# Performance work log

Hardware: AMD Instinct MI355X
Metric: run time of the kernel (lower is better)

Reference implementation:

```python
import jax, jax.numpy as jnp
import numpy as np


def setup_inputs() -> dict:
    key = jax.random.key(0)
    ks = jax.random.split(key, 5)
    B, S, H, I = 8, 2048, 1024, 4096
    # int8 quantized activation / weights / int8 bias, held as int32 for portability
    hidden_states = jax.random.randint(ks[0], (B, S, H), -128, 128, dtype=jnp.int32)
    w_fc = jax.random.randint(ks[1], (H, I), -128, 128, dtype=jnp.int32)   # Conv1D weight [in, out]
    b_fc = jax.random.randint(ks[2], (I,), -128, 128, dtype=jnp.int32)     # int8 bias (B8)
    w_proj = jax.random.randint(ks[3], (I, H), -128, 128, dtype=jnp.int32)
    b_proj = jax.random.normal(ks[4], (H,), dtype=jnp.float32)             # fp32 bias (BFP32)
    alpha_fc = jnp.float32(0.004)   # (x_scale * w_scale / out_scale) of c_fc
    beta_fc = jnp.float32(0.02)     # bias_scale / out_scale of c_fc
    alpha_proj = jnp.float32(0.003) # x_scale * w_scale of c_proj (dequant to fp32)
    return {
        "hidden_states": hidden_states,
        "w_fc": w_fc, "b_fc": b_fc, "alpha_fc": alpha_fc, "beta_fc": beta_fc,
        "w_proj": w_proj, "b_proj": b_proj, "alpha_proj": alpha_proj,
    }


def reference(hidden_states, w_fc, b_fc, alpha_fc, beta_fc, w_proj, b_proj, alpha_proj):
    # ---- c_fc: W8A8B8O8 Conv1D + fused ReLU + requantization to int8 ----
    acc1 = jnp.matmul(hidden_states, w_fc)                       # [B,S,I] int32
    h = acc1.astype(jnp.float32) * alpha_fc + b_fc.astype(jnp.float32) * beta_fc
    h = jax.nn.relu(h)
    # requantize to int8 (round + saturate)
    h_q = jnp.clip(jnp.round(h), -128.0, 127.0).astype(jnp.int32)  # [B,S,I]
    # ---- c_proj: W8A8BFP32OFP32 Conv1D (dequant to fp32) ----
    acc2 = jnp.matmul(h_q, w_proj)                               # [B,S,H] int32
    out = acc2.astype(jnp.float32) * alpha_proj + b_proj
    # dropout is identity in eval mode
    return out
```

## Files before the change

kernel.cpp:

```cpp
#include <hip/hip_runtime.h>
#include <cstdint>
#include <cstddef>

typedef int int4v __attribute__((ext_vector_type(4)));
typedef signed char schar;

#define DEVI __device__ __forceinline__

DEVI void load_lds16(const void* g, void* l) {
  __builtin_amdgcn_global_load_lds(
      (const __attribute__((address_space(1))) void*)g,
      (__attribute__((address_space(3))) void*)l, 16, 0, 0);
}

#define BAR() __builtin_amdgcn_s_barrier()
#define LGKM0()                                                     \
  do {                                                              \
    asm volatile("s_waitcnt lgkmcnt(0)" ::: "memory");              \
    __builtin_amdgcn_sched_barrier(0);                              \
  } while (0)
#define VMW(n)                                                      \
  do {                                                              \
    asm volatile("s_waitcnt vmcnt(" #n ")" ::: "memory");           \
    __builtin_amdgcn_sched_barrier(0);                              \
  } while (0)

__global__ __launch_bounds__(256) void pack_i8(const int* __restrict__ src,
                                               signed char* __restrict__ dst,
                                               int n4) {
  int i = blockIdx.x * 256 + threadIdx.x;
  if (i >= n4) return;
  int4v v = ((const int4v*)src)[i];
  int p = (v.x & 255) | ((v.y & 255) << 8) | ((v.z & 255) << 16) | (v.w << 24);
  ((int*)dst)[i] = p;
}

__global__ __launch_bounds__(256) void pack_wT(const int* __restrict__ w,
                                               signed char* __restrict__ wT,
                                               int K, int N) {
  __shared__ signed char t[64][68];
  int n0 = blockIdx.x * 64, k0 = blockIdx.y * 64;
  int tr = threadIdx.x >> 6, tc = threadIdx.x & 63;
#pragma unroll
  for (int i = 0; i < 16; ++i) {
    int r = i * 4 + tr;
    t[r][tc] = (signed char)w[(size_t)(k0 + r) * N + n0 + tc];
  }
  __syncthreads();
#pragma unroll
  for (int i = 0; i < 16; ++i) {
    int r = i * 4 + tr;
    wT[(size_t)(n0 + r) * K + k0 + tc] = t[tc][r];
  }
}

template <int EPI>
__global__ __launch_bounds__(512, 2) void gemm8(
    const schar* __restrict__ A, const schar* __restrict__ BT,
    int M, int N, int K, const int* __restrict__ bias_i,
    const float* __restrict__ alphaP, const float* __restrict__ betaP,
    const float* __restrict__ bias_f, schar* __restrict__ outQ,
    float* __restrict__ outF) {
  extern __shared__ schar lds[];
  constexpr int ATILE = 32768;

  const int tid = threadIdx.x;
  const int wid = tid >> 6, lane = tid & 63;
  const int wr = wid >> 2, wc = wid & 3;
  const int l16 = lane & 15, l4 = lane >> 4;

  const int gx = gridDim.x;
  const int nwg = gx * gridDim.y;
  const int bid = blockIdx.y * gx + blockIdx.x;
  const int swz = (bid & 7) * (nwg >> 3) + (bid >> 3);
  const int rowBase = (swz / gx) * 256;
  const int colBase = (swz % gx) * 256;

  const int NT = K >> 7;

  const int off0 = tid * 16, off1 = 8192 + tid * 16;
  const int rl0 = off0 >> 7, rl1 = off1 >> 7;
  const int gs0 = ((off0 >> 4) & 7) ^ (rl0 & 7);
  const int gs1 = ((off1 >> 4) & 7) ^ (rl1 & 7);
  const schar* gA0 = A + (size_t)(rowBase + rl0) * K + gs0 * 16;
  const schar* gA1 = A + (size_t)(rowBase + rl1) * K + gs1 * 16;
  const schar* gB0 = BT + (size_t)(colBase + rl0) * K + gs0 * 16;
  const schar* gB1 = BT + (size_t)(colBase + rl1) * K + gs1 * 16;
  const size_t hstep = (size_t)128 * K;
  const int wb = wid * 1024;

  auto stA = [&](int buf, int t, int h) {
    schar* d = lds + buf * ATILE + h * 16384 + wb;
    load_lds16(gA0 + (size_t)t * 128 + (size_t)h * hstep, d);
    load_lds16(gA1 + (size_t)t * 128 + (size_t)h * hstep, d + 8192);
  };
  auto stB = [&](int buf, int t, int h) {
    schar* d = lds + 2 * ATILE + buf * ATILE + h * 16384 + wb;
    load_lds16(gB0 + (size_t)t * 128 + (size_t)h * hstep, d);
    load_lds16(gB1 + (size_t)t * 128 + (size_t)h * hstep, d + 8192);
  };

  int4v acc[8][4] = {};
  int4v a[4][2], b0[2][2], b1[2][2];

#define LDA(QM, Ab)                                                         \
  do {                                                                      \
    _Pragma("unroll") for (int mi = 0; mi < 4; ++mi)                        \
        _Pragma("unroll") for (int kk = 0; kk < 2; ++kk) a[mi][kk] =        \
        *(const int4v*)((Ab) + (wr * 128 + (QM)*64 + mi * 16 + l16) * 128 + \
                        (((kk * 4) + l4) ^ (l16 & 7)) * 16);                \
  } while (0)
#define LDB(B, QN, Bb)                                                       \
  do {                                                                       \
    _Pragma("unroll") for (int ni = 0; ni < 2; ++ni)                         \
        _Pragma("unroll") for (int kk = 0; kk < 2; ++kk) (B)[ni][kk] =       \
        *(const int4v*)((Bb) +                                               \
                        (wc * 64 + ((QN)*2 + ni) * 16 + l16) * 128 +         \
                        (((kk * 4) + l4) ^ (l16 & 7)) * 16);                 \
  } while (0)
#define MMQ(QM, QN, B)                                                       \
  do {                                                                       \
    __builtin_amdgcn_s_setprio(1);                                           \
    _Pragma("unroll") for (int kk = 0; kk < 2; ++kk)                         \
        _Pragma("unroll") for (int mi = 0; mi < 4; ++mi)                     \
            _Pragma("unroll") for (int ni = 0; ni < 2; ++ni)                 \
                acc[(QM)*4 + mi][(QN)*2 + ni] =                              \
        __builtin_amdgcn_mfma_i32_16x16x64_i8(                               \
            a[mi][kk], (B)[ni][kk], acc[(QM)*4 + mi][(QN)*2 + ni], 0, 0, 0); \
    __builtin_amdgcn_s_setprio(0);                                           \
  } while (0)

  stA(0, 0, 0);
  stA(0, 0, 1);
  stB(0, 0, 0);
  stB(0, 0, 1);
  if (NT > 1) {
    stB(1, 1, 0);
    stB(1, 1, 1);
    VMW(4);
  } else {
    VMW(0);
  }
  BAR();

  for (int T = 0; T < NT; ++T) {
    const int cb = T & 1, ob = cb ^ 1;
    const schar* Ac = lds + cb * ATILE;
    const schar* Bc = lds + 2 * ATILE + cb * ATILE;

    LDA(0, Ac);
    LDB(b0, 0, Bc);
    if (T + 1 < NT) stA(ob, T + 1, 0);
    BAR();
    LGKM0();
    MMQ(0, 0, b0);
    BAR();
    LDB(b1, 1, Bc);
    if (T + 1 < NT) stA(ob, T + 1, 1);
    BAR();
    LGKM0();
    MMQ(0, 1, b1);
    BAR();
    LDA(1, Ac);
    if (T + 2 < NT) stB(cb, T + 2, 0);
    BAR();
    LGKM0();
    MMQ(1, 0, b0);
    BAR();
    if (T + 2 < NT) stB(cb, T + 2, 1);
    BAR();
    MMQ(1, 1, b1);
    if (T + 2 < NT) {
      VMW(4);
    } else if (T + 1 < NT) {
      VMW(0);
    }
    BAR();
  }

  const float alpha = alphaP[0];
  if (EPI == 0) {
    const float beta = betaP[0];
#pragma unroll
    for (int MI = 0; MI < 8; ++MI) {
      int row = rowBase + wr * 128 + MI * 16 + l4 * 4;
#pragma unroll
      for (int NI = 0; NI < 4; ++NI) {
        int col = colBase + wc * 64 + NI * 16 + l16;
        float bt = (float)bias_i[col] * beta;
#pragma unroll
        for (int j = 0; j < 4; ++j) {
          float h = (float)acc[MI][NI][j] * alpha + bt;
          h = fmaxf(h, 0.f);
          h = rintf(h);
          h = fminf(h, 127.f);
          outQ[(size_t)(row + j) * N + col] = (schar)h;
        }
      }
    }
  } else {
#pragma unroll
    for (int MI = 0; MI < 8; ++MI) {
      int row = rowBase + wr * 128 + MI * 16 + l4 * 4;
#pragma unroll
      for (int NI = 0; NI < 4; ++NI) {
        int col = colBase + wc * 64 + NI * 16 + l16;
        float bv = bias_f[col];
#pragma unroll
        for (int j = 0; j < 4; ++j) {
          outF[(size_t)(row + j) * N + col] =
              (float)acc[MI][NI][j] * alpha + bv;
        }
      }
    }
  }
#undef LDA
#undef LDB
#undef MMQ
}

extern "C" void kernel_launch(void* const* d_in, const int* in_sizes, int n_in,
                              void* d_out, int out_size, void* d_ws,
                              size_t ws_size, hipStream_t stream) {
  const int M = 16384, H = 1024, I = 4096;
  const int* hidden = (const int*)d_in[0];
  const int* w_fc = (const int*)d_in[1];
  const int* b_fc = (const int*)d_in[2];
  const float* alpha_fc = (const float*)d_in[3];
  const float* beta_fc = (const float*)d_in[4];
  const int* w_proj = (const int*)d_in[5];
  const float* b_proj = (const float*)d_in[6];
  const float* alpha_proj = (const float*)d_in[7];
  float* out = (float*)d_out;

  signed char* hq = (signed char*)d_ws;
  signed char* aP = hq + (size_t)M * I;
  signed char* wfcT = aP + (size_t)M * H;
  signed char* wpT = wfcT + (size_t)I * H;

  hipFuncSetAttribute((const void*)gemm8<0>,
                      hipFuncAttributeMaxDynamicSharedMemorySize, 131072);
  hipFuncSetAttribute((const void*)gemm8<1>,
                      hipFuncAttributeMaxDynamicSharedMemorySize, 131072);

  pack_i8<<<(M * H / 4 + 255) / 256, 256, 0, stream>>>(hidden, aP, M * H / 4);
  pack_wT<<<dim3(I / 64, H / 64), 256, 0, stream>>>(w_fc, wfcT, H, I);
  pack_wT<<<dim3(H / 64, I / 64), 256, 0, stream>>>(w_proj, wpT, I, H);

  gemm8<0><<<dim3(I / 256, M / 256), 512, 131072, stream>>>(
      aP, wfcT, M, I, H, b_fc, alpha_fc, beta_fc, nullptr, hq, nullptr);
  gemm8<1><<<dim3(H / 256, M / 256), 512, 131072, stream>>>(
      hq, wpT, M, H, I, nullptr, alpha_proj, nullptr, b_proj, nullptr, out);
}
```

Baseline: 178.9 us.

## Double-buffer A fragments and prefetch next tile's LDS reads across MFMA phases

```diff
diff --git a/kernel.cpp b/kernel.cpp
--- a/kernel.cpp
+++ b/kernel.cpp
@@ -13,16 +13,17 @@
       (__attribute__((address_space(3))) void*)l, 16, 0, 0);
 }
 
+#define SB0() __builtin_amdgcn_sched_barrier(0)
 #define BAR() __builtin_amdgcn_s_barrier()
-#define LGKM0()                                                     \
-  do {                                                              \
-    asm volatile("s_waitcnt lgkmcnt(0)" ::: "memory");              \
-    __builtin_amdgcn_sched_barrier(0);                              \
-  } while (0)
-#define VMW(n)                                                      \
-  do {                                                              \
-    asm volatile("s_waitcnt vmcnt(" #n ")" ::: "memory");           \
-    __builtin_amdgcn_sched_barrier(0);                              \
+#define LGKM(n)                                                   \
+  do {                                                            \
+    asm volatile("s_waitcnt lgkmcnt(" #n ")" ::: "memory");       \
+    SB0();                                                        \
+  } while (0)
+#define VMW(n)                                                    \
+  do {                                                            \
+    asm volatile("s_waitcnt vmcnt(" #n ")" ::: "memory");         \
+    SB0();                                                        \
   } while (0)
 
 __global__ __launch_bounds__(256) void pack_i8(const int* __restrict__ src,
@@ -77,6 +78,11 @@
   const int colBase = (swz % gx) * 256;
 
   const int NT = K >> 7;
+
+  const float alpha = alphaP[0];
+  const float beta = (EPI == 0) ? betaP[0] : 0.f;
+  asm volatile("" ::"s"(alpha), "s"(beta));
+  LGKM(0);
 
   const int off0 = tid * 16, off1 = 8192 + tid * 16;
   const int rl0 = off0 >> 7, rl1 = off1 >> 7;
@@ -101,24 +107,23 @@
   };
 
   int4v acc[8][4] = {};
-  int4v a[4][2], b0[2][2], b1[2][2];
-
-#define LDA(QM, Ab)                                                         \
+  int4v aA[4][2], aB[4][2], b0[2][2], b1[2][2];
+
+#define LDA(DST, QM, Ab)                                                    \
   do {                                                                      \
     _Pragma("unroll") for (int mi = 0; mi < 4; ++mi)                        \
-        _Pragma("unroll") for (int kk = 0; kk < 2; ++kk) a[mi][kk] =        \
+        _Pragma("unroll") for (int kk = 0; kk < 2; ++kk) (DST)[mi][kk] =    \
         *(const int4v*)((Ab) + (wr * 128 + (QM)*64 + mi * 16 + l16) * 128 + \
                         (((kk * 4) + l4) ^ (l16 & 7)) * 16);                \
   } while (0)
-#define LDB(B, QN, Bb)                                                       \
+#define LDB(DST, QN, Bb)                                                     \
   do {                                                                       \
     _Pragma("unroll") for (int ni = 0; ni < 2; ++ni)                         \
-        _Pragma("unroll") for (int kk = 0; kk < 2; ++kk) (B)[ni][kk] =       \
-        *(const int4v*)((Bb) +                                               \
-                        (wc * 64 + ((QN)*2 + ni) * 16 + l16) * 128 +         \
+        _Pragma("unroll") for (int kk = 0; kk < 2; ++kk) (DST)[ni][kk] =     \
+        *(const int4v*)((Bb) + (wc * 64 + ((QN)*2 + ni) * 16 + l16) * 128 +  \
                         (((kk * 4) + l4) ^ (l16 & 7)) * 16);                 \
   } while (0)
-#define MMQ(QM, QN, B)                                                       \
+#define MMQ(QM, QN, AF, BF)                                                  \
   do {                                                                       \
     __builtin_amdgcn_s_setprio(1);                                           \
     _Pragma("unroll") for (int kk = 0; kk < 2; ++kk)                         \
@@ -126,7 +131,8 @@
             _Pragma("unroll") for (int ni = 0; ni < 2; ++ni)                 \
                 acc[(QM)*4 + mi][(QN)*2 + ni] =                              \
         __builtin_amdgcn_mfma_i32_16x16x64_i8(                               \
-            a[mi][kk], (B)[ni][kk], acc[(QM)*4 + mi][(QN)*2 + ni], 0, 0, 0); \
+            (AF)[mi][kk], (BF)[ni][kk], acc[(QM)*4 + mi][(QN)*2 + ni], 0, 0, \
+            0);                                                              \
     __builtin_amdgcn_s_setprio(0);                                           \
   } while (0)
 
@@ -134,53 +140,63 @@
   stA(0, 0, 1);
   stB(0, 0, 0);
   stB(0, 0, 1);
-  if (NT > 1) {
-    stB(1, 1, 0);
-    stB(1, 1, 1);
-    VMW(4);
-  } else {
-    VMW(0);
-  }
+  stB(1, 1, 0);
+  stB(1, 1, 1);
+  VMW(4);
   BAR();
+  SB0();
+  LDA(aA, 0, lds);
+  LDB(b0, 0, lds + 2 * ATILE);
+  SB0();
 
   for (int T = 0; T < NT; ++T) {
     const int cb = T & 1, ob = cb ^ 1;
     const schar* Ac = lds + cb * ATILE;
     const schar* Bc = lds + 2 * ATILE + cb * ATILE;
-
-    LDA(0, Ac);
-    LDB(b0, 0, Bc);
+    const schar* An = lds + ob * ATILE;
+    const schar* Bn = lds + 2 * ATILE + ob * ATILE;
+
+    LDA(aB, 1, Ac);
+    LDB(b1, 1, Bc);
     if (T + 1 < NT) stA(ob, T + 1, 0);
-    BAR();
-    LGKM0();
-    MMQ(0, 0, b0);
-    BAR();
-    LDB(b1, 1, Bc);
+    SB0();
+    BAR();
+    LGKM(12);
+    MMQ(0, 0, aA, b0);
+    SB0();
+    BAR();
     if (T + 1 < NT) stA(ob, T + 1, 1);
-    BAR();
-    LGKM0();
-    MMQ(0, 1, b1);
-    BAR();
-    LDA(1, Ac);
-    if (T + 2 < NT) stB(cb, T + 2, 0);
-    BAR();
-    LGKM0();
-    MMQ(1, 0, b0);
-    BAR();
+    SB0();
+    BAR();
+    LGKM(4);
+    MMQ(1, 0, aB, b0);
+    LGKM(0);
+    SB0();
+    BAR();
+    if (T + 2 < NT) {
+      stB(cb, T + 2, 0);
+      VMW(2);
+    } else {
+      VMW(0);
+    }
+    SB0();
+    BAR();
+    MMQ(0, 1, aA, b1);
+    SB0();
+    BAR();
+    if (T + 1 < NT) {
+      LDA(aA, 0, An);
+      LDB(b0, 0, Bn);
+    }
     if (T + 2 < NT) stB(cb, T + 2, 1);
-    BAR();
-    MMQ(1, 1, b1);
-    if (T + 2 < NT) {
-      VMW(4);
-    } else if (T + 1 < NT) {
-      VMW(0);
-    }
-    BAR();
-  }
-
-  const float alpha = alphaP[0];
+    SB0();
+    BAR();
+    MMQ(1, 1, aB, b1);
+    SB0();
+    BAR();
+  }
+
   if (EPI == 0) {
-    const float beta = betaP[0];
 #pragma unroll
     for (int MI = 0; MI < 8; ++MI) {
       int row = rowBase + wr * 128 + MI * 16 + l4 * 4;
```

Result: no change. 181.3 us (+1.4%).
